# Kernel tuning notes

Hardware: AMD Instinct MI355X
Metric: run time of the kernel (lower is better)

Reference implementation:

```python
import jax, jax.numpy as jnp
import numpy as np

HIDDEN = 1024
HEADS = 16
HEAD_DIM = HIDDEN // HEADS

def setup_inputs() -> dict:
    key = jax.random.key(0)
    ks = jax.random.split(key, 11)
    B, T, D = 2, 2048, HIDDEN
    s = 1.0 / np.sqrt(D)
    return {
        "query": jax.random.normal(ks[0], (B, T, D), jnp.float32),
        "key": jax.random.normal(ks[1], (B, T, D), jnp.float32),
        "value": jax.random.normal(ks[2], (B, T, D), jnp.float32),
        "Wq": jax.random.normal(ks[3], (D, D), jnp.float32) * s,
        "bq": jnp.zeros((D,), jnp.float32),
        "Wk": jax.random.normal(ks[4], (D, D), jnp.float32) * s,
        "bk": jnp.zeros((D,), jnp.float32),
        "Wv": jax.random.normal(ks[5], (D, D), jnp.float32) * s,
        "bv": jnp.zeros((D,), jnp.float32),
        "Wo": jax.random.normal(ks[6], (D, D), jnp.float32) * s,
        "bo": jnp.zeros((D,), jnp.float32),
    }

def reference(query, key, value, Wq, bq, Wk, bk, Wv, bv, Wo, bo):
    B, Tq, D = query.shape
    Tk = key.shape[1]
    H, Hd = HEADS, HEAD_DIM
    # projections -> [B, H, T, Hd]
    Q = (query @ Wq + bq).reshape(B, Tq, H, Hd).transpose(0, 2, 1, 3)
    K = (key @ Wk + bk).reshape(B, Tk, H, Hd).transpose(0, 2, 1, 3)
    V = (value @ Wv + bv).reshape(B, Tk, H, Hd).transpose(0, 2, 1, 3)
    scale = jnp.sqrt(jnp.asarray(Hd, Q.dtype))
    scores = jnp.einsum('bhqd,bhkd->bhqk', Q, K) / scale  # [B,H,Tq,Tk]
    causal = jnp.triu(jnp.ones((Tq, Tk), bool), k=1)
    scores = jnp.where(causal[None, None], jnp.asarray(-jnp.inf, scores.dtype), scores)
    attn = jax.nn.softmax(scores, axis=-1)
    out = jnp.einsum('bhqk,bhkd->bhqd', attn, V)  # [B,H,Tq,Hd]
    out = out.transpose(0, 2, 1, 3).reshape(B, Tq, D)
    return out @ Wo + bo
```

## Files before the change

kernel.cpp:

```cpp
#include <hip/hip_runtime.h>
#include <hip/hip_bf16.h>


typedef __bf16 bf16_t;
typedef __bf16 bf16x4 __attribute__((ext_vector_type(4)));
typedef __bf16 bf16x8 __attribute__((ext_vector_type(8)));
typedef float f32x4 __attribute__((ext_vector_type(4)));
typedef float f32x16 __attribute__((ext_vector_type(16)));
typedef unsigned int u32;
typedef unsigned int u32x2v __attribute__((ext_vector_type(2)));
typedef unsigned int u32x4v __attribute__((ext_vector_type(4)));

#define D_MODEL 1024
#define SEQ_T   2048
#define NHEAD   16
#define HDIM    64
#define M_ROWS  4096
#define MEGA    (1024 * 1024)

__device__ __forceinline__ void gl2lds16(const void* g, void* l) {
    __builtin_amdgcn_global_load_lds((const __attribute__((address_space(1))) u32*)g,
                                     (__attribute__((address_space(3))) u32*)l, 16, 0, 0);
}

__device__ __forceinline__ u32 pk2(float a, float b) {
    unsigned short x = __builtin_bit_cast(unsigned short, (bf16_t)a);
    unsigned short y = __builtin_bit_cast(unsigned short, (bf16_t)b);
    return (u32)x | ((u32)y << 16);
}

#define JOB4(j, k0, n, s, m) ((j) | ((k0) << 4) | ((n) << 10) | ((s) << 14) | ((m) << 19))
__device__ __constant__ int JOBS4[34] = {
    JOB4(4, 0, 10, 0, 0),
    JOB4(9, 0, 10, 8, 1),  JOB4(9, 10, 10, 9, 1),
    JOB4(13, 0, 10, 19, 1),
    JOB4(14, 0, 10, 22, 1), JOB4(14, 10, 10, 23, 1), JOB4(14, 20, 10, 24, 1),
    JOB4(8, 0, 9, 6, 1),   JOB4(8, 9, 9, 7, 1),
    JOB4(12, 0, 9, 16, 1), JOB4(12, 9, 9, 17, 1),
    JOB4(13, 10, 9, 20, 1), JOB4(13, 19, 9, 21, 1),
    JOB4(3, 0, 8, 0, 0),
    JOB4(7, 0, 8, 4, 1),   JOB4(7, 8, 8, 5, 1),
    JOB4(10, 0, 8, 10, 1),
    JOB4(11, 0, 8, 13, 1), JOB4(11, 8, 8, 14, 1), JOB4(11, 16, 8, 15, 1),
    JOB4(12, 18, 8, 18, 1),
    JOB4(15, 0, 8, 25, 1), JOB4(15, 8, 8, 26, 1), JOB4(15, 16, 8, 27, 1), JOB4(15, 24, 8, 28, 1),
    JOB4(6, 0, 7, 2, 1),   JOB4(6, 7, 7, 3, 1),
    JOB4(10, 8, 7, 11, 1), JOB4(10, 15, 7, 12, 1),
    JOB4(2, 0, 6, 0, 0),
    JOB4(5, 0, 6, 0, 1),   JOB4(5, 6, 6, 1, 1),
    JOB4(1, 0, 4, 0, 0),
    JOB4(0, 0, 2, 0, 0)
};
__device__ __constant__ int CMB4[11] = {
    5 | (2 << 4) | (0 << 8),  6 | (2 << 4) | (2 << 8),  7 | (2 << 4) | (4 << 8),
    8 | (2 << 4) | (6 << 8),  9 | (2 << 4) | (8 << 8),  10 | (3 << 4) | (10 << 8),
    11 | (3 << 4) | (13 << 8), 12 | (3 << 4) | (16 << 8), 13 | (3 << 4) | (19 << 8),
    14 | (3 << 4) | (22 << 8), 15 | (4 << 4) | (25 << 8)
};
#define SLOTS_PER_BH 29
#define SLOT_F       8320
#define SLOTS_IN_A   504

__device__ __forceinline__ float* slot_ptr(float* PwA, float* PwB, int s) {
    return s < SLOTS_IN_A ? PwA + (size_t)s * SLOT_F
                          : PwB + (size_t)(s - SLOTS_IN_A) * SLOT_F;
}

__global__ __launch_bounds__(256) void prep(
    const float* __restrict__ Wq, const float* __restrict__ Wk,
    const float* __restrict__ Wv, const float* __restrict__ Wo,
    const float* __restrict__ Xq, const float* __restrict__ Xk, const float* __restrict__ Xv,
    bf16_t* __restrict__ Wqt, bf16_t* __restrict__ Wkt,
    bf16_t* __restrict__ Wvt, bf16_t* __restrict__ Wot,
    bf16_t* __restrict__ Xb)
{
    int blk = blockIdx.x, tid = threadIdx.x;
    if (blk < 4096) {
        int wi = blk >> 10, t = blk & 1023;
        int n0 = (t & 31) * 32, k0 = (t >> 5) * 32;
        const float* W = wi == 0 ? Wq : (wi == 1 ? Wk : (wi == 2 ? Wv : Wo));
        bf16_t* Wt = wi == 0 ? Wqt : (wi == 1 ? Wkt : (wi == 2 ? Wvt : Wot));
        __shared__ float tile[32][33];
        int tx = tid & 31, ty = tid >> 5;
#pragma unroll
        for (int i = 0; i < 32; i += 8)
            tile[ty + i][tx] = W[(k0 + ty + i) * D_MODEL + n0 + tx];
        __syncthreads();
#pragma unroll
        for (int i = 0; i < 32; i += 8)
            Wt[(size_t)(n0 + ty + i) * D_MODEL + k0 + tx] = (bf16_t)tile[tx][ty + i];
    } else {
        int b2 = blk - 4096;
        int xi = b2 >> 10;
        const float* X = xi == 0 ? Xq : (xi == 1 ? Xk : Xv);
        bf16_t* XB = Xb + (size_t)xi * M_ROWS * D_MODEL;
        size_t base = (size_t)(b2 & 1023) * 4096 + tid * 16;
        const float4* xp = (const float4*)(X + base);
        float4 a0 = xp[0], a1 = xp[1], a2 = xp[2], a3 = xp[3];
        bf16x8 o0, o1;
        o0[0] = (bf16_t)a0.x; o0[1] = (bf16_t)a0.y; o0[2] = (bf16_t)a0.z; o0[3] = (bf16_t)a0.w;
        o0[4] = (bf16_t)a1.x; o0[5] = (bf16_t)a1.y; o0[6] = (bf16_t)a1.z; o0[7] = (bf16_t)a1.w;
        o1[0] = (bf16_t)a2.x; o1[1] = (bf16_t)a2.y; o1[2] = (bf16_t)a2.z; o1[3] = (bf16_t)a2.w;
        o1[4] = (bf16_t)a3.x; o1[5] = (bf16_t)a3.y; o1[6] = (bf16_t)a3.z; o1[7] = (bf16_t)a3.w;
        *(bf16x8*)(XB + base) = o0;
        *(bf16x8*)(XB + base + 8) = o1;
    }
}

template <bool PRECAST>
__global__ __launch_bounds__(256) void proj_fused(
    const float* __restrict__ Xq, const float* __restrict__ Xk, const float* __restrict__ Xv,
    const bf16_t* __restrict__ Xb,
    const bf16_t* __restrict__ Wqt, const bf16_t* __restrict__ Wkt, const bf16_t* __restrict__ Wvt,
    const float* __restrict__ bq, const float* __restrict__ bk, const float* __restrict__ bv,
    bf16_t* __restrict__ Qh, bf16_t* __restrict__ Kh, bf16_t* __restrict__ Vt)
{
    __shared__ bf16_t Ab[128 * 32];
    __shared__ bf16_t Bb[128 * 32];
    int tid = threadIdx.x;
    int w = tid >> 6, lane = tid & 63, lo16 = lane & 15, quad = lane >> 4;
    int m0 = blockIdx.x * 128;
    int proj = blockIdx.y >> 3;
    int n0 = (blockIdx.y & 7) * 128;
    const float*  X    = proj == 0 ? Xq  : (proj == 1 ? Xk  : Xv);
    const bf16_t* XB   = Xb + (size_t)proj * M_ROWS * D_MODEL;
    const bf16_t* Wt   = proj == 0 ? Wqt : (proj == 1 ? Wkt : Wvt);
    const float*  bias = proj == 0 ? bq  : (proj == 1 ? bk  : bv);
    int wm = (w >> 1) * 64, wn = (w & 1) * 64;

    f32x4 acc[4][4];
#pragma unroll
    for (int i = 0; i < 4; i++)
#pragma unroll
        for (int j = 0; j < 4; j++) acc[i][j] = (f32x4){0.f, 0.f, 0.f, 0.f};

    for (int k0 = 0; k0 < D_MODEL; k0 += 32) {
        __syncthreads();
#pragma unroll
        for (int p = 0; p < 2; p++) {
            int idx = p * 256 + tid;
            int row = idx >> 2, ch = (idx & 3) * 8;
            if (PRECAST) {
                gl2lds16(XB + (size_t)(m0 + row) * D_MODEL + k0 + ch, Ab + idx * 8);
            } else {
                const float* as = X + (size_t)(m0 + row) * D_MODEL + k0 + ch;
                float4 a0 = *(const float4*)as, a1 = *(const float4*)(as + 4);
                bf16x8 av;
                av[0] = (bf16_t)a0.x; av[1] = (bf16_t)a0.y; av[2] = (bf16_t)a0.z; av[3] = (bf16_t)a0.w;
                av[4] = (bf16_t)a1.x; av[5] = (bf16_t)a1.y; av[6] = (bf16_t)a1.z; av[7] = (bf16_t)a1.w;
                *(bf16x8*)(Ab + idx * 8) = av;
            }
            gl2lds16(Wt + (size_t)(n0 + row) * D_MODEL + k0 + ch, Bb + idx * 8);
        }
        __syncthreads();
        bf16x8 af[4], bfr[4];
#pragma unroll
        for (int i = 0; i < 4; i++)
            af[i] = *(bf16x8*)(Ab + (wm + i * 16 + lo16) * 32 + quad * 8);
#pragma unroll
        for (int j = 0; j < 4; j++)
            bfr[j] = *(bf16x8*)(Bb + (wn + j * 16 + lo16) * 32 + quad * 8);
#pragma unroll
        for (int i = 0; i < 4; i++)
#pragma unroll
            for (int j = 0; j < 4; j++)
                acc[i][j] = __builtin_amdgcn_mfma_f32_16x16x32_bf16(af[i], bfr[j], acc[i][j], 0, 0, 0);
    }

    float qscale = proj == 0 ? 0.1803368801111244f : 1.0f;
#pragma unroll
    for (int j = 0; j < 4; j++) {
        int col = n0 + wn + j * 16 + lo16;
        float bv2 = bias[col];
        int h = col >> 6, hd = col & 63;
#pragma unroll
        for (int i = 0; i < 4; i++) {
#pragma unroll
            for (int r = 0; r < 4; r++) {
                int m = m0 + wm + i * 16 + quad * 4 + r;
                int b = m >> 11, t = m & 2047;
                bf16_t val = (bf16_t)((acc[i][j][r] + bv2) * qscale);
                if (proj == 2)
                    Vt[(((size_t)(b * NHEAD + h) * HDIM + hd) * SEQ_T) + t] = val;
                else if (proj == 1)
                    Kh[(((size_t)(b * NHEAD + h) * SEQ_T + t) * HDIM) + hd] = val;
                else
                    Qh[(((size_t)(b * NHEAD + h) * SEQ_T + t) * HDIM) + hd] = val;
            }
        }
    }
}

__global__ __launch_bounds__(256, 2) void flash_attn(const bf16_t* __restrict__ Qh,
                                                     const bf16_t* __restrict__ Kh,
                                                     const bf16_t* __restrict__ Vt,
                                                     bf16_t* __restrict__ Ob,
                                                     float* __restrict__ PwA,
                                                     float* __restrict__ PwB) {
    int blk = blockIdx.x;
    int bh = blk & 31;
    int enc = JOBS4[blk >> 5];
    int j4 = enc & 15, kt0 = (enc >> 4) & 63, nkt = (enc >> 10) & 15;
    int slot = (enc >> 14) & 31, multi = (enc >> 19) & 1;
    int tid = threadIdx.x;
    int w = tid >> 6, lane = tid & 63;
    int l32 = lane & 31, hi = lane >> 5;
    int qbase = j4 * 128 + w * 32;
    int diagkt = 2 * j4 + (w >> 1);

    __shared__ bf16_t KL[2][64 * 64];
    __shared__ bf16_t VL[2][64 * 64];

    const bf16_t* Qp = Qh + (size_t)bh * SEQ_T * HDIM;
    const bf16_t* Kp = Kh + (size_t)bh * SEQ_T * HDIM;
    const bf16_t* Vp = Vt + (size_t)bh * HDIM * SEQ_T;

    bf16x8 qf[4];
    {
        const bf16_t* qr = Qp + (size_t)(qbase + l32) * HDIM;
#pragma unroll
        for (int kd = 0; kd < 4; kd++)
            qf[kd] = *(const bf16x8*)(qr + kd * 16 + hi * 8);
    }

    bf16x8 ones;
#pragma unroll
    for (int i = 0; i < 8; i++) ones[i] = (bf16_t)1.0f;

    f32x16 oacc[2], lacc;
#pragma unroll
    for (int r = 0; r < 16; r++) { oacc[0][r] = 0.f; oacc[1][r] = 0.f; lacc[r] = 0.f; }

#pragma unroll
    for (int p = 0; p < 2; p++) {
        int idx = p * 256 + tid;
        int row = idx >> 3, cp = idx & 7, cl = (cp - row) & 7;
        gl2lds16(Kp + (size_t)(kt0 * 64 + row) * HDIM + cl * 8, KL[0] + idx * 8);
        gl2lds16(Vp + (size_t)row * SEQ_T + kt0 * 64 + cl * 8, VL[0] + idx * 8);
    }

    for (int it = 0; it < nkt; it++) {
        int kt = kt0 + it;
        int cur = it & 1;
        __syncthreads();

        if (it + 1 < nkt) {
#pragma unroll
            for (int p = 0; p < 2; p++) {
                int idx = p * 256 + tid;
                int row = idx >> 3, cp = idx & 7, cl = (cp - row) & 7;
                gl2lds16(Kp + (size_t)((kt + 1) * 64 + row) * HDIM + cl * 8, KL[cur ^ 1] + idx * 8);
                gl2lds16(Vp + (size_t)row * SEQ_T + (kt + 1) * 64 + cl * 8, VL[cur ^ 1] + idx * 8);
            }
        }
        if (kt > diagkt) continue;
        const bf16_t* KLc = KL[cur];
        const bf16_t* VLc = VL[cur];

        f32x16 sacc[2];
#pragma unroll
        for (int r = 0; r < 16; r++) { sacc[0][r] = 0.f; sacc[1][r] = 0.f; }
        __builtin_amdgcn_s_setprio(1);
#pragma unroll
        for (int ks = 0; ks < 2; ks++) {
            int key = l32 + 32 * ks;
#pragma unroll
            for (int kd = 0; kd < 4; kd++) {
                bf16x8 kf = *(const bf16x8*)(KLc + key * 64 + ((2 * kd + hi + key) & 7) * 8);
                sacc[ks] = __builtin_amdgcn_mfma_f32_32x32x16_bf16(kf, qf[kd], sacc[ks], 0, 0, 0);
            }
        }
        __builtin_amdgcn_s_setprio(0);

        bool diag = (kt == diagkt);
        int qg = qbase + l32;
#pragma unroll
        for (int ks = 0; ks < 2; ks++)
#pragma unroll
            for (int r = 0; r < 16; r++) {
                float e = exp2f(sacc[ks][r]);
                if (diag) {
                    int key = kt * 64 + ks * 32 + (r & 3) + 8 * (r >> 2) + 4 * hi;
                    e = (key <= qg) ? e : 0.f;
                }
                sacc[ks][r] = e;
            }

        bf16x8 pf[4];
#pragma unroll
        for (int t = 0; t < 4; t++) {
            const int ks = t >> 1, bb = (t & 1) * 8;
            u32 A1 = pk2(sacc[ks][bb + 0], sacc[ks][bb + 1]);
            u32 A2 = pk2(sacc[ks][bb + 2], sacc[ks][bb + 3]);
            u32 C1 = pk2(sacc[ks][bb + 4], sacc[ks][bb + 5]);
            u32 C2 = pk2(sacc[ks][bb + 6], sacc[ks][bb + 7]);
            u32x2v s1 = __builtin_amdgcn_permlane32_swap(A1, C1, false, false);
            u32x2v s2 = __builtin_amdgcn_permlane32_swap(A2, C2, false, false);
            u32x4v wv; wv[0] = s1[0]; wv[1] = s2[0]; wv[2] = s1[1]; wv[3] = s2[1];
            pf[t] = __builtin_bit_cast(bf16x8, wv);
            lacc = __builtin_amdgcn_mfma_f32_32x32x16_bf16(pf[t], ones, lacc, 0, 0, 0);
        }

        __builtin_amdgcn_s_setprio(1);
#pragma unroll
        for (int dt = 0; dt < 2; dt++) {
            int d = l32 + 32 * dt;
#pragma unroll
            for (int t = 0; t < 4; t++) {
                bf16x8 vf = *(const bf16x8*)(VLc + d * 64 + ((2 * t + hi + d) & 7) * 8);
                oacc[dt] = __builtin_amdgcn_mfma_f32_32x32x16_bf16(pf[t], vf, oacc[dt], 0, 0, 0);
            }
        }
        __builtin_amdgcn_s_setprio(0);
    }

    if (multi) {
        float* sp = slot_ptr(PwA, PwB, bh * SLOTS_PER_BH + slot);
#pragma unroll
        for (int dt = 0; dt < 2; dt++)
#pragma unroll
            for (int r = 0; r < 16; r++) {
                int qrow = w * 32 + (r & 3) + 8 * (r >> 2) + 4 * hi;
                sp[qrow * 64 + l32 + 32 * dt] = oacc[dt][r];
            }
        if (l32 == 0) {
#pragma unroll
            for (int r = 0; r < 16; r++)
                sp[8192 + w * 32 + (r & 3) + 8 * (r >> 2) + 4 * hi] = lacc[r];
        }
    } else {
        int b = bh >> 4, h = bh & 15;
        float inv[16];
#pragma unroll
        for (int r = 0; r < 16; r++) inv[r] = 1.0f / lacc[r];
#pragma unroll
        for (int dt = 0; dt < 2; dt++)
#pragma unroll
            for (int r = 0; r < 16; r++) {
                int q = qbase + (r & 3) + 8 * (r >> 2) + 4 * hi;
                int d = l32 + 32 * dt;
                Ob[((size_t)b * SEQ_T + q) * D_MODEL + h * HDIM + d] = (bf16_t)(oacc[dt][r] * inv[r]);
            }
    }
}

__global__ __launch_bounds__(256) void combine(float* __restrict__ PwA,
                                               float* __restrict__ PwB,
                                               bf16_t* __restrict__ Ob) {
    int blk = blockIdx.x;
    int bh = blk / 11, e = blk % 11;
    int info = CMB4[e];
    int j4 = info & 15, c = (info >> 4) & 7, base = info >> 8;
    int s0 = bh * SLOTS_PER_BH + base;
    int b = bh >> 4, h = bh & 15;
    int tid = threadIdx.x;
    __shared__ float linv[128];
    if (tid < 128) {
        float s = 0.f;
        for (int k = 0; k < c; k++) s += slot_ptr(PwA, PwB, s0 + k)[8192 + tid];
        linv[tid] = 1.0f / s;
    }
    __syncthreads();
#pragma unroll
    for (int i = 0; i < 8; i++) {
        int e4 = i * 1024 + tid * 4;
        f32x4 a = (f32x4){0.f, 0.f, 0.f, 0.f};
        for (int k = 0; k < c; k++) {
            f32x4 v = *(const f32x4*)(slot_ptr(PwA, PwB, s0 + k) + e4);
            a[0] += v[0]; a[1] += v[1]; a[2] += v[2]; a[3] += v[3];
        }
        int q = e4 >> 6, d = e4 & 63;
        float il = linv[q];
        bf16x4 o;
        o[0] = (bf16_t)(a[0] * il); o[1] = (bf16_t)(a[1] * il);
        o[2] = (bf16_t)(a[2] * il); o[3] = (bf16_t)(a[3] * il);
        *(bf16x4*)(Ob + ((size_t)b * SEQ_T + j4 * 128 + q) * D_MODEL + h * HDIM + d) = o;
    }
}

__global__ __launch_bounds__(256) void out_gemm(const bf16_t* __restrict__ A,
                                                const bf16_t* __restrict__ Wt,
                                                const float* __restrict__ bias,
                                                float* __restrict__ out) {
    __shared__ bf16_t Ab[128 * 32];
    __shared__ bf16_t Bb[128 * 32];
    int tid = threadIdx.x;
    int w = tid >> 6, lane = tid & 63, lo16 = lane & 15, quad = lane >> 4;
    int m0 = blockIdx.x * 128;
    int n0 = blockIdx.y * 128;
    int wm = (w >> 1) * 64, wn = (w & 1) * 64;

    f32x4 acc[4][4];
#pragma unroll
    for (int i = 0; i < 4; i++)
#pragma unroll
        for (int j = 0; j < 4; j++) acc[i][j] = (f32x4){0.f, 0.f, 0.f, 0.f};

    for (int k0 = 0; k0 < D_MODEL; k0 += 32) {
        __syncthreads();
#pragma unroll
        for (int p = 0; p < 2; p++) {
            int idx = p * 256 + tid;
            int row = idx >> 2, ch = (idx & 3) * 8;
            gl2lds16(A  + (size_t)(m0 + row) * D_MODEL + k0 + ch, Ab + idx * 8);
            gl2lds16(Wt + (size_t)(n0 + row) * D_MODEL + k0 + ch, Bb + idx * 8);
        }
        __syncthreads();
        bf16x8 af[4], bfr[4];
#pragma unroll
        for (int i = 0; i < 4; i++)
            af[i] = *(bf16x8*)(Ab + (wm + i * 16 + lo16) * 32 + quad * 8);
#pragma unroll
        for (int j = 0; j < 4; j++)
            bfr[j] = *(bf16x8*)(Bb + (wn + j * 16 + lo16) * 32 + quad * 8);
#pragma unroll
        for (int i = 0; i < 4; i++)
#pragma unroll
            for (int j = 0; j < 4; j++)
                acc[i][j] = __builtin_amdgcn_mfma_f32_16x16x32_bf16(af[i], bfr[j], acc[i][j], 0, 0, 0);
    }

#pragma unroll
    for (int j = 0; j < 4; j++) {
        int col = n0 + wn + j * 16 + lo16;
        float bv2 = bias[col];
#pragma unroll
        for (int i = 0; i < 4; i++)
#pragma unroll
            for (int r = 0; r < 4; r++) {
                int m = m0 + wm + i * 16 + quad * 4 + r;
                out[(size_t)m * D_MODEL + col] = acc[i][j][r] + bv2;
            }
    }
}

extern "C" void kernel_launch(void* const* d_in, const int* in_sizes, int n_in,
                              void* d_out, int out_size, void* d_ws, size_t ws_size,
                              hipStream_t stream) {
    const float* q  = (const float*)d_in[0];
    const float* k  = (const float*)d_in[1];
    const float* v  = (const float*)d_in[2];
    const float* Wq = (const float*)d_in[3];
    const float* bq = (const float*)d_in[4];
    const float* Wk = (const float*)d_in[5];
    const float* bk = (const float*)d_in[6];
    const float* Wv = (const float*)d_in[7];
    const float* bv = (const float*)d_in[8];
    const float* Wo = (const float*)d_in[9];
    const float* bo = (const float*)d_in[10];
    float* out = (float*)d_out;

    bf16_t* Wqt = (bf16_t*)d_ws;
    bf16_t* Wkt = Wqt + (size_t)MEGA;
    bf16_t* Wvt = Wkt + (size_t)MEGA;
    bf16_t* Wot = Wvt + (size_t)MEGA;
    bf16_t* Qh  = Wot + (size_t)MEGA;
    bf16_t* Kh  = Qh  + (size_t)M_ROWS * D_MODEL;
    bf16_t* Vt  = Kh  + (size_t)M_ROWS * D_MODEL;
    bf16_t* Xb  = Vt  + (size_t)M_ROWS * D_MODEL;
    bf16_t* Ob  = Xb;
    float*  PwA = (float*)(Xb + (size_t)M_ROWS * D_MODEL);
    bf16_t* ws_end = Xb + (size_t)3 * M_ROWS * D_MODEL;

    size_t used_bytes = (size_t)(4 * MEGA + 6 * M_ROWS * D_MODEL) * sizeof(bf16_t);
    size_t pwb_bytes  = (size_t)(928 - SLOTS_IN_A) * SLOT_F * sizeof(float);
    float* PwB = (ws_size >= used_bytes + pwb_bytes) ? (float*)ws_end : (float*)d_out;

    bool precast = ws_size >= used_bytes;

    int prep_blocks = precast ? 4096 + 3 * 1024 : 4096;
    prep<<<prep_blocks, 256, 0, stream>>>(Wq, Wk, Wv, Wo, q, k, v, Wqt, Wkt, Wvt, Wot, Xb);

    dim3 pg(M_ROWS / 128, 24);
    if (precast)
        proj_fused<true><<<pg, 256, 0, stream>>>(q, k, v, Xb, Wqt, Wkt, Wvt, bq, bk, bv, Qh, Kh, Vt);
    else
        proj_fused<false><<<pg, 256, 0, stream>>>(q, k, v, Xb, Wqt, Wkt, Wvt, bq, bk, bv, Qh, Kh, Vt);

    flash_attn<<<34 * 32, 256, 0, stream>>>(Qh, Kh, Vt, Ob, PwA, PwB);
    combine<<<11 * 32, 256, 0, stream>>>(PwA, PwB, Ob);

    dim3 og(M_ROWS / 128, D_MODEL / 128);
    out_gemm<<<og, 256, 0, stream>>>(Ob, Wot, bo, out);
}
```

Baseline: 235.0 us.

## Double-buffer LDS tiles and swizzle layout in projection and output GEMMs

```diff
diff --git a/kernel.cpp b/kernel.cpp
--- a/kernel.cpp
+++ b/kernel.cpp
@@ -115,8 +115,8 @@
     const float* __restrict__ bq, const float* __restrict__ bk, const float* __restrict__ bv,
     bf16_t* __restrict__ Qh, bf16_t* __restrict__ Kh, bf16_t* __restrict__ Vt)
 {
-    __shared__ bf16_t Ab[128 * 32];
-    __shared__ bf16_t Bb[128 * 32];
+    __shared__ bf16_t Ab[2][128 * 32];
+    __shared__ bf16_t Bb[2][128 * 32];
     int tid = threadIdx.x;
     int w = tid >> 6, lane = tid & 63, lo16 = lane & 15, quad = lane >> 4;
     int m0 = blockIdx.x * 128;
@@ -134,38 +134,55 @@
 #pragma unroll
         for (int j = 0; j < 4; j++) acc[i][j] = (f32x4){0.f, 0.f, 0.f, 0.f};
 
+#define PROJ_STAGE(K0, BUF)                                                         \
+    {                                                                               \
+        _Pragma("unroll")                                                           \
+        for (int p = 0; p < 2; p++) {                                               \
+            int idx = p * 256 + tid;                                                \
+            int row = idx >> 2, cp = idx & 3, cl = (cp - row) & 3;                  \
+            if (PRECAST) {                                                          \
+                gl2lds16(XB + (size_t)(m0 + row) * D_MODEL + (K0) + cl * 8,         \
+                         Ab[BUF] + idx * 8);                                        \
+            } else {                                                                \
+                const float* as = X + (size_t)(m0 + row) * D_MODEL + (K0) + cl * 8; \
+                float4 a0 = *(const float4*)as, a1 = *(const float4*)(as + 4);      \
+                bf16x8 av;                                                          \
+                av[0] = (bf16_t)a0.x; av[1] = (bf16_t)a0.y;                         \
+                av[2] = (bf16_t)a0.z; av[3] = (bf16_t)a0.w;                         \
+                av[4] = (bf16_t)a1.x; av[5] = (bf16_t)a1.y;                         \
+                av[6] = (bf16_t)a1.z; av[7] = (bf16_t)a1.w;                         \
+                *(bf16x8*)(Ab[BUF] + idx * 8) = av;                                 \
+            }                                                                       \
+            gl2lds16(Wt + (size_t)(n0 + row) * D_MODEL + (K0) + cl * 8,             \
+                     Bb[BUF] + idx * 8);                                            \
+        }                                                                           \
+    }
+
+    PROJ_STAGE(0, 0);
+
     for (int k0 = 0; k0 < D_MODEL; k0 += 32) {
+        int cur = (k0 >> 5) & 1;
         __syncthreads();
-#pragma unroll
-        for (int p = 0; p < 2; p++) {
-            int idx = p * 256 + tid;
-            int row = idx >> 2, ch = (idx & 3) * 8;
-            if (PRECAST) {
-                gl2lds16(XB + (size_t)(m0 + row) * D_MODEL + k0 + ch, Ab + idx * 8);
-            } else {
-                const float* as = X + (size_t)(m0 + row) * D_MODEL + k0 + ch;
-                float4 a0 = *(const float4*)as, a1 = *(const float4*)(as + 4);
-                bf16x8 av;
-                av[0] = (bf16_t)a0.x; av[1] = (bf16_t)a0.y; av[2] = (bf16_t)a0.z; av[3] = (bf16_t)a0.w;
-                av[4] = (bf16_t)a1.x; av[5] = (bf16_t)a1.y; av[6] = (bf16_t)a1.z; av[7] = (bf16_t)a1.w;
-                *(bf16x8*)(Ab + idx * 8) = av;
-            }
-            gl2lds16(Wt + (size_t)(n0 + row) * D_MODEL + k0 + ch, Bb + idx * 8);
-        }
-        __syncthreads();
+        if (k0 + 32 < D_MODEL) PROJ_STAGE(k0 + 32, cur ^ 1);
+
         bf16x8 af[4], bfr[4];
 #pragma unroll
-        for (int i = 0; i < 4; i++)
-            af[i] = *(bf16x8*)(Ab + (wm + i * 16 + lo16) * 32 + quad * 8);
-#pragma unroll
-        for (int j = 0; j < 4; j++)
-            bfr[j] = *(bf16x8*)(Bb + (wn + j * 16 + lo16) * 32 + quad * 8);
+        for (int i = 0; i < 4; i++) {
+            int R = wm + i * 16 + lo16;
+            af[i] = *(bf16x8*)(Ab[cur] + R * 32 + ((quad + R) & 3) * 8);
+        }
+#pragma unroll
+        for (int j = 0; j < 4; j++) {
+            int R = wn + j * 16 + lo16;
+            bfr[j] = *(bf16x8*)(Bb[cur] + R * 32 + ((quad + R) & 3) * 8);
+        }
 #pragma unroll
         for (int i = 0; i < 4; i++)
 #pragma unroll
             for (int j = 0; j < 4; j++)
                 acc[i][j] = __builtin_amdgcn_mfma_f32_16x16x32_bf16(af[i], bfr[j], acc[i][j], 0, 0, 0);
     }
+#undef PROJ_STAGE
 
     float qscale = proj == 0 ? 0.1803368801111244f : 1.0f;
 #pragma unroll
@@ -382,8 +399,8 @@
                                                 const bf16_t* __restrict__ Wt,
                                                 const float* __restrict__ bias,
                                                 float* __restrict__ out) {
-    __shared__ bf16_t Ab[128 * 32];
-    __shared__ bf16_t Bb[128 * 32];
+    __shared__ bf16_t Ab[2][128 * 32];
+    __shared__ bf16_t Bb[2][128 * 32];
     int tid = threadIdx.x;
     int w = tid >> 6, lane = tid & 63, lo16 = lane & 15, quad = lane >> 4;
     int m0 = blockIdx.x * 128;
@@ -396,29 +413,44 @@
 #pragma unroll
         for (int j = 0; j < 4; j++) acc[i][j] = (f32x4){0.f, 0.f, 0.f, 0.f};
 
+#define OUT_STAGE(K0, BUF)                                                      \
+    {                                                                           \
+        _Pragma("unroll")                                                       \
+        for (int p = 0; p < 2; p++) {                                           \
+            int idx = p * 256 + tid;                                            \
+            int row = idx >> 2, cp = idx & 3, cl = (cp - row) & 3;              \
+            gl2lds16(A  + (size_t)(m0 + row) * D_MODEL + (K0) + cl * 8,         \
+                     Ab[BUF] + idx * 8);                                        \
+            gl2lds16(Wt + (size_t)(n0 + row) * D_MODEL + (K0) + cl * 8,         \
+                     Bb[BUF] + idx * 8);                                        \
+        }                                                                       \
+    }
+
+    OUT_STAGE(0, 0);
+
     for (int k0 = 0; k0 < D_MODEL; k0 += 32) {
+        int cur = (k0 >> 5) & 1;
         __syncthreads();
-#pragma unroll
-        for (int p = 0; p < 2; p++) {
-            int idx = p * 256 + tid;
-            int row = idx >> 2, ch = (idx & 3) * 8;
-            gl2lds16(A  + (size_t)(m0 + row) * D_MODEL + k0 + ch, Ab + idx * 8);
-            gl2lds16(Wt + (size_t)(n0 + row) * D_MODEL + k0 + ch, Bb + idx * 8);
-        }
-        __syncthreads();
+        if (k0 + 32 < D_MODEL) OUT_STAGE(k0 + 32, cur ^ 1);
+
         bf16x8 af[4], bfr[4];
 #pragma unroll
-        for (int i = 0; i < 4; i++)
-            af[i] = *(bf16x8*)(Ab + (wm + i * 16 + lo16) * 32 + quad * 8);
-#pragma unroll
-        for (int j = 0; j < 4; j++)
-            bfr[j] = *(bf16x8*)(Bb + (wn + j * 16 + lo16) * 32 + quad * 8);
+        for (int i = 0; i < 4; i++) {
+            int R = wm + i * 16 + lo16;
+            af[i] = *(bf16x8*)(Ab[cur] + R * 32 + ((quad + R) & 3) * 8);
+        }
+#pragma unroll
+        for (int j = 0; j < 4; j++) {
+            int R = wn + j * 16 + lo16;
+            bfr[j] = *(bf16x8*)(Bb[cur] + R * 32 + ((quad + R) & 3) * 8);
+        }
 #pragma unroll
         for (int i = 0; i < 4; i++)
 #pragma unroll
             for (int j = 0; j < 4; j++)
                 acc[i][j] = __builtin_amdgcn_mfma_f32_16x16x32_bf16(af[i], bfr[j], acc[i][j], 0, 0, 0);
     }
+#undef OUT_STAGE
 
 #pragma unroll
     for (int j = 0; j < 4; j++) {
```

New measurement: 235.0 us. About the same (-0.0%).
